# Optimization experiments

Measured on AMD Instinct MI355X. Metric: run time of the kernel, lower is better.

The kernel has to match this reference:

```python
import jax, jax.numpy as jnp
import numpy as np

B, T, C, H = 8, 2048, 1024, 64  # batch, seq (== block_size), n_embd, head_size


def setup_inputs() -> dict:
    key = jax.random.key(0)
    k1, k2, k3, k4 = jax.random.split(key, 4)
    x = jax.random.normal(k1, (B, T, C), dtype=jnp.float32)
    scale = 0.02
    Wk = jax.random.normal(k2, (H, C), dtype=jnp.float32) * scale  # nn.Linear weight [out,in]
    Wq = jax.random.normal(k3, (H, C), dtype=jnp.float32) * scale
    Wv = jax.random.normal(k4, (H, C), dtype=jnp.float32) * scale
    return {"x": x, "Wk": Wk, "Wq": Wq, "Wv": Wv}


def reference(x, Wk, Wq, Wv):
    # k, q, v projections (bias-free linears): x @ W.T
    k = jnp.einsum('btc,hc->bth', x, Wk)
    q = jnp.einsum('btc,hc->bth', x, Wq)
    v = jnp.einsum('btc,hc->bth', x, Wv)
    # NOTE: source MULTIPLIES by sqrt(head_size) (faithful to original code)
    wei = jnp.einsum('bth,bsh->bts', q, k) * (H ** 0.5)  # [B,T,T]
    causal = jnp.tril(jnp.ones((T, T), dtype=bool))
    wei = jnp.where(causal, wei, -jnp.inf)
    wei = jax.nn.softmax(wei, axis=-1)
    # dropout_value = 0.0 -> identity (deterministic baseline)
    out = jnp.einsum('bts,bsh->bth', wei, v)  # [B,T,H]
    return out
```

## Files before the change

kernel.cpp:

```cpp
#include <hip/hip_runtime.h>

#define BB 8
#define TT 2048
#define CC 1024
#define HH 64
#define MM (BB * TT)

typedef _Float16 half8 __attribute__((ext_vector_type(8)));
typedef _Float16 half4 __attribute__((ext_vector_type(4)));
typedef float floatx4 __attribute__((ext_vector_type(4)));

template <int CTRL>
__device__ __forceinline__ float dpp_max_step(float x)
{
    union { float f; int i; } u, v;
    u.f = x;
    v.i = __builtin_amdgcn_update_dpp(u.i, u.i, CTRL, 0xf, 0xf, false);
    return fmaxf(x, v.f);
}
__device__ __forceinline__ float rowmax16(float x)
{
    x = dpp_max_step<0x128>(x);
    x = dpp_max_step<0x124>(x);
    x = dpp_max_step<0x122>(x);
    x = dpp_max_step<0x121>(x);
    return x;
}

__global__ __launch_bounds__(256)
void w_convert(const float* __restrict__ Wk, const float* __restrict__ Wq,
               const float* __restrict__ Wv, _Float16* __restrict__ W16)
{
    const int e = (blockIdx.x * 256 + threadIdx.x) * 8;
    const int row = e >> 10;
    const int c   = e & 1023;
    const int which = row >> 6;
    const float* __restrict__ src = (which == 0) ? Wq : ((which == 1) ? Wk : Wv);
    const float scale = (which == 0) ? 8.0f : 1.0f;
    const int srow = row & 63;
    const float4 a = *reinterpret_cast<const float4*>(&src[srow * 1024 + c]);
    const float4 b = *reinterpret_cast<const float4*>(&src[srow * 1024 + c + 4]);
    const half8 o = { (_Float16)(a.x * scale), (_Float16)(a.y * scale),
                      (_Float16)(a.z * scale), (_Float16)(a.w * scale),
                      (_Float16)(b.x * scale), (_Float16)(b.y * scale),
                      (_Float16)(b.z * scale), (_Float16)(b.w * scale) };
    *reinterpret_cast<half8*>(&W16[e]) = o;
}

__device__ __forceinline__ void qkv_loadA(const float* __restrict__ xrow, int k0,
                                          float4& xa, float4& xb)
{
    xa = *reinterpret_cast<const float4*>(xrow + k0);
    xb = *reinterpret_cast<const float4*>(xrow + k0 + 4);
}
__device__ __forceinline__ void qkv_loadB(const _Float16* __restrict__ wbase, int k0,
                                          half8 (&bf)[12])
{
    #pragma unroll
    for (int n = 0; n < 12; ++n)
        bf[n] = *reinterpret_cast<const half8*>(wbase + (size_t)n * 16 * CC + k0);
}
__device__ __forceinline__ void qkv_mfma(const float4& xa, const float4& xb,
                                         const half8 (&bf)[12], floatx4 (&acc)[12])
{
    const half8 af = { (_Float16)xa.x, (_Float16)xa.y, (_Float16)xa.z, (_Float16)xa.w,
                       (_Float16)xb.x, (_Float16)xb.y, (_Float16)xb.z, (_Float16)xb.w };
    #pragma unroll
    for (int n = 0; n < 12; ++n)
        acc[n] = __builtin_amdgcn_mfma_f32_16x16x32_f16(af, bf[n], acc[n], 0, 0, 0);
}

__global__ __launch_bounds__(256, 1)
void qkv_direct(const float* __restrict__ x, const _Float16* __restrict__ W16,
                _Float16* __restrict__ q16, _Float16* __restrict__ k16,
                _Float16* __restrict__ vt16)
{
    const int tid  = threadIdx.x;
    const int lane = tid & 63;
    const int wv   = tid >> 6;
    const int tile = blockIdx.x * 4 + wv;
    const int m_base = tile * 16;
    const int fm = lane & 15;
    const int fq = lane >> 4;
    const int fk = fq * 8;
    const int fr = fq * 4;

    const float*     __restrict__ xrow  = &x[(size_t)(m_base + fm) * CC + fk];
    const _Float16*  __restrict__ wbase = &W16[(size_t)fm * CC + fk];

    floatx4 acc[12];
    #pragma unroll
    for (int n = 0; n < 12; ++n)
        #pragma unroll
        for (int r = 0; r < 4; ++r) acc[n][r] = 0.0f;

    float4 xa0, xb0, xa1, xb1;
    half8 bf0[12], bf1[12];

    qkv_loadA(xrow, 0, xa0, xb0);
    qkv_loadB(wbase, 0, bf0);

    #pragma unroll 2
    for (int c = 0; c < 32; c += 2) {
        qkv_loadA(xrow, (c + 1) * 32, xa1, xb1);
        qkv_loadB(wbase, (c + 1) * 32, bf1);
        qkv_mfma(xa0, xb0, bf0, acc);
        if (c + 2 < 32) {
            qkv_loadA(xrow, (c + 2) * 32, xa0, xb0);
            qkv_loadB(wbase, (c + 2) * 32, bf0);
        }
        qkv_mfma(xa1, xb1, bf1, acc);
    }

    const int b  = m_base >> 11;
    const int t0 = m_base & 2047;
    #pragma unroll
    for (int n = 0; n < 12; ++n) {
        const int col = n * 16 + fm;
        if (n < 8) {
            _Float16* __restrict__ dst = (n < 4) ? q16 : k16;
            const int h = col & 63;
            #pragma unroll
            for (int r = 0; r < 4; ++r)
                dst[(size_t)(m_base + fr + r) * HH + h] = (_Float16)acc[n][r];
        } else {
            const int h = col - 128;
            const half4 pk = { (_Float16)acc[n][0], (_Float16)acc[n][1],
                               (_Float16)acc[n][2], (_Float16)acc[n][3] };
            *reinterpret_cast<half4*>(
                &vt16[((size_t)b * HH + h) * TT + t0 + fr]) = pk;
        }
    }
}

__global__ __launch_bounds__(128, 3)
void attn(const _Float16* __restrict__ q16, const _Float16* __restrict__ k16,
          const _Float16* __restrict__ vt16, float* __restrict__ out)
{
    __shared__ _Float16 Ks[64 * 72];
    __shared__ _Float16 Vts[64 * 72];
    __shared__ _Float16 Ps[2 * 16 * 72];

    const int bid = blockIdx.x;
    const int b = bid & 7;
    const int g = bid >> 3;
    const int it = (g < 32) ? (63 - g) : (g - 32);
    const int tid  = threadIdx.x;
    const int lane = tid & 63;
    const int wv   = tid >> 6;
    const int fm   = lane & 15;
    const int fk   = (lane >> 4) * 8;
    const int fr   = (lane >> 4) * 4;

    const _Float16* __restrict__ qb  = q16  + (size_t)b * TT * HH;
    const _Float16* __restrict__ kb  = k16  + (size_t)b * TT * HH;
    const _Float16* __restrict__ vtb = vt16 + (size_t)b * HH * TT;

    const int qrow = it * 32 + wv * 16 + fm;
    const half8 qf0 = *reinterpret_cast<const half8*>(&qb[(size_t)qrow * HH + fk]);
    const half8 qf1 = *reinterpret_cast<const half8*>(&qb[(size_t)qrow * HH + 32 + fk]);

    floatx4 O[4], lacc;
    float m_r[4];
    #pragma unroll
    for (int r = 0; r < 4; ++r) {
        m_r[r] = -3.0e38f;
        lacc[r] = 0.0f;
        #pragma unroll
        for (int ht = 0; ht < 4; ++ht) O[ht][r] = 0.0f;
    }

    const half8 ones = { (_Float16)1.f, (_Float16)1.f, (_Float16)1.f, (_Float16)1.f,
                         (_Float16)1.f, (_Float16)1.f, (_Float16)1.f, (_Float16)1.f };

    const int Ji = (it >> 1) + 1;
    const int sr = tid >> 3;
    const int sc = (tid & 7) * 8;

    half8 kr[4], vr[4];
    #pragma unroll
    for (int i = 0; i < 4; ++i) {
        kr[i] = *reinterpret_cast<const half8*>(&kb[(size_t)(sr + i * 16) * HH + sc]);
        vr[i] = *reinterpret_cast<const half8*>(&vtb[(size_t)(sr + i * 16) * TT + sc]);
    }

    for (int j = 0; j < Ji; ++j) {
        __syncthreads();
        #pragma unroll
        for (int i = 0; i < 4; ++i) {
            *reinterpret_cast<half8*>(&Ks[(sr + i * 16) * 72 + sc])  = kr[i];
            *reinterpret_cast<half8*>(&Vts[(sr + i * 16) * 72 + sc]) = vr[i];
        }
        __syncthreads();

        if (j + 1 < Ji) {
            const int jn = (j + 1) * 64;
            #pragma unroll
            for (int i = 0; i < 4; ++i) {
                kr[i] = *reinterpret_cast<const half8*>(&kb[(size_t)(jn + sr + i * 16) * HH + sc]);
                vr[i] = *reinterpret_cast<const half8*>(&vtb[(size_t)(sr + i * 16) * TT + jn + sc]);
            }
        }

        floatx4 sa[4];
        #pragma unroll
        for (int nt = 0; nt < 4; ++nt) {
            #pragma unroll
            for (int r = 0; r < 4; ++r) sa[nt][r] = 0.0f;
            const _Float16* kp = &Ks[(nt * 16 + fm) * 72];
            const half8 b0 = *reinterpret_cast<const half8*>(kp + fk);
            const half8 b1 = *reinterpret_cast<const half8*>(kp + 32 + fk);
            sa[nt] = __builtin_amdgcn_mfma_f32_16x16x32_f16(qf0, b0, sa[nt], 0, 0, 0);
            sa[nt] = __builtin_amdgcn_mfma_f32_16x16x32_f16(qf1, b1, sa[nt], 0, 0, 0);
        }

        if (j == Ji - 1) {
            const int rbase = it * 32 + wv * 16 + fr;
            #pragma unroll
            for (int nt = 0; nt < 4; ++nt) {
                const int col = j * 64 + nt * 16 + fm;
                #pragma unroll
                for (int r = 0; r < 4; ++r)
                    if (col > rbase + r) sa[nt][r] = -3.0e38f;
            }
        }

        #pragma unroll
        for (int r = 0; r < 4; ++r) {
            float mx = fmaxf(fmaxf(sa[0][r], sa[1][r]), fmaxf(sa[2][r], sa[3][r]));
            mx = rowmax16(mx);
            const float mn = fmaxf(m_r[r], mx);
            const float alpha = __expf(m_r[r] - mn);
            m_r[r] = mn;
            _Float16* pp = &Ps[wv * 1152 + (fr + r) * 72 + fm];
            pp[0]  = (_Float16)__expf(sa[0][r] - mn);
            pp[16] = (_Float16)__expf(sa[1][r] - mn);
            pp[32] = (_Float16)__expf(sa[2][r] - mn);
            pp[48] = (_Float16)__expf(sa[3][r] - mn);
            lacc[r] *= alpha;
            O[0][r] *= alpha; O[1][r] *= alpha; O[2][r] *= alpha; O[3][r] *= alpha;
        }
        __syncthreads();

        #pragma unroll
        for (int ch = 0; ch < 2; ++ch) {
            const half8 pa = *reinterpret_cast<const half8*>(
                &Ps[wv * 1152 + fm * 72 + ch * 32 + fk]);
            lacc = __builtin_amdgcn_mfma_f32_16x16x32_f16(pa, ones, lacc, 0, 0, 0);
            #pragma unroll
            for (int ht = 0; ht < 4; ++ht) {
                const half8 vb = *reinterpret_cast<const half8*>(
                    &Vts[(ht * 16 + fm) * 72 + ch * 32 + fk]);
                O[ht] = __builtin_amdgcn_mfma_f32_16x16x32_f16(pa, vb, O[ht], 0, 0, 0);
            }
        }
    }

    #pragma unroll
    for (int r = 0; r < 4; ++r) {
        const float inv = 1.0f / lacc[r];
        const size_t rowoff = (size_t)(b * TT + it * 32 + wv * 16 + fr + r) * HH;
        #pragma unroll
        for (int ht = 0; ht < 4; ++ht)
            out[rowoff + ht * 16 + fm] = O[ht][r] * inv;
    }
}

extern "C" void kernel_launch(void* const* d_in, const int* in_sizes, int n_in,
                              void* d_out, int out_size, void* d_ws, size_t ws_size,
                              hipStream_t stream)
{
    (void)in_sizes; (void)n_in; (void)out_size; (void)ws_size;

    const float* x  = (const float*)d_in[0];
    const float* Wk = (const float*)d_in[1];
    const float* Wq = (const float*)d_in[2];
    const float* Wv = (const float*)d_in[3];
    float* out = (float*)d_out;

    _Float16* q16  = (_Float16*)d_ws;
    _Float16* k16  = q16 + (size_t)MM * HH;
    _Float16* vt16 = k16 + (size_t)MM * HH;
    _Float16* W16  = vt16 + (size_t)MM * HH;

    w_convert<<<dim3(96), dim3(256), 0, stream>>>(Wk, Wq, Wv, W16);
    qkv_direct<<<dim3(256), dim3(256), 0, stream>>>(x, W16, q16, k16, vt16);
    attn<<<dim3(512), dim3(128), 0, stream>>>(q16, k16, vt16, out);
}
```

Baseline: 182.4 us.

## Split QKV projection across wave pairs and make attention waves independent

The projection kernel now gives each wave half of the 192 output columns for a 16-row tile. It stages the x tile through per-wave LDS as fp16, in 64-wide K chunks, and runs twice as many blocks. The attention kernel drops the shared K/V LDS tiles, the prefetch registers and all block barriers. Each wave independently handles a 16-row query tile and reads K and V^T straight from global memory, relying on caches. This removes barrier and LDS staging overhead and raises parallelism. In exchange it loses cross-wave K/V reuse, drops the causal load-balancing order, and may leave tail imbalance and more global and L2 traffic.

```diff
diff --git a/kernel.cpp b/kernel.cpp
--- a/kernel.cpp
+++ b/kernel.cpp
@@ -47,78 +47,63 @@
     *reinterpret_cast<half8*>(&W16[e]) = o;
 }
 
-__device__ __forceinline__ void qkv_loadA(const float* __restrict__ xrow, int k0,
-                                          float4& xa, float4& xb)
-{
-    xa = *reinterpret_cast<const float4*>(xrow + k0);
-    xb = *reinterpret_cast<const float4*>(xrow + k0 + 4);
-}
-__device__ __forceinline__ void qkv_loadB(const _Float16* __restrict__ wbase, int k0,
-                                          half8 (&bf)[12])
-{
-    #pragma unroll
-    for (int n = 0; n < 12; ++n)
-        bf[n] = *reinterpret_cast<const half8*>(wbase + (size_t)n * 16 * CC + k0);
-}
-__device__ __forceinline__ void qkv_mfma(const float4& xa, const float4& xb,
-                                         const half8 (&bf)[12], floatx4 (&acc)[12])
-{
-    const half8 af = { (_Float16)xa.x, (_Float16)xa.y, (_Float16)xa.z, (_Float16)xa.w,
-                       (_Float16)xb.x, (_Float16)xb.y, (_Float16)xb.z, (_Float16)xb.w };
-    #pragma unroll
-    for (int n = 0; n < 12; ++n)
-        acc[n] = __builtin_amdgcn_mfma_f32_16x16x32_f16(af, bf[n], acc[n], 0, 0, 0);
-}
-
-__global__ __launch_bounds__(256, 1)
-void qkv_direct(const float* __restrict__ x, const _Float16* __restrict__ W16,
-                _Float16* __restrict__ q16, _Float16* __restrict__ k16,
-                _Float16* __restrict__ vt16)
-{
+__global__ __launch_bounds__(256, 2)
+void qkv2(const float* __restrict__ x, const _Float16* __restrict__ W16,
+          _Float16* __restrict__ q16, _Float16* __restrict__ k16,
+          _Float16* __restrict__ vt16)
+{
+    __shared__ _Float16 Xs[4 * 16 * 68];
+
     const int tid  = threadIdx.x;
     const int lane = tid & 63;
     const int wv   = tid >> 6;
-    const int tile = blockIdx.x * 4 + wv;
-    const int m_base = tile * 16;
+    const int gw   = blockIdx.x * 4 + wv;
+    const int mtile = gw >> 1;
+    const int nh    = gw & 1;
     const int fm = lane & 15;
     const int fq = lane >> 4;
     const int fk = fq * 8;
     const int fr = fq * 4;
-
-    const float*     __restrict__ xrow  = &x[(size_t)(m_base + fm) * CC + fk];
-    const _Float16*  __restrict__ wbase = &W16[(size_t)fm * CC + fk];
-
-    floatx4 acc[12];
-    #pragma unroll
-    for (int n = 0; n < 12; ++n)
+    const int m_base = mtile * 16;
+
+    _Float16* __restrict__ Xw = &Xs[wv * 16 * 68];
+    const _Float16* __restrict__ wb = &W16[(size_t)(nh * 96 + fm) * CC + fk];
+
+    floatx4 acc[6];
+    #pragma unroll
+    for (int n = 0; n < 6; ++n)
         #pragma unroll
         for (int r = 0; r < 4; ++r) acc[n][r] = 0.0f;
 
-    float4 xa0, xb0, xa1, xb1;
-    half8 bf0[12], bf1[12];
-
-    qkv_loadA(xrow, 0, xa0, xb0);
-    qkv_loadB(wbase, 0, bf0);
-
-    #pragma unroll 2
-    for (int c = 0; c < 32; c += 2) {
-        qkv_loadA(xrow, (c + 1) * 32, xa1, xb1);
-        qkv_loadB(wbase, (c + 1) * 32, bf1);
-        qkv_mfma(xa0, xb0, bf0, acc);
-        if (c + 2 < 32) {
-            qkv_loadA(xrow, (c + 2) * 32, xa0, xb0);
-            qkv_loadB(wbase, (c + 2) * 32, bf0);
-        }
-        qkv_mfma(xa1, xb1, bf1, acc);
+    for (int k0 = 0; k0 < CC; k0 += 64) {
+        #pragma unroll
+        for (int i = 0; i < 4; ++i) {
+            const float4 xv = *reinterpret_cast<const float4*>(
+                &x[(size_t)(m_base + i * 4 + fq) * CC + k0 + fm * 4]);
+            const half4 h = { (_Float16)xv.x, (_Float16)xv.y,
+                              (_Float16)xv.z, (_Float16)xv.w };
+            *reinterpret_cast<half4*>(&Xw[(i * 4 + fq) * 68 + fm * 4]) = h;
+        }
+        const half8 af0 = *reinterpret_cast<const half8*>(&Xw[fm * 68 + fk]);
+        const half8 af1 = *reinterpret_cast<const half8*>(&Xw[fm * 68 + 32 + fk]);
+
+        #pragma unroll
+        for (int n = 0; n < 6; ++n) {
+            const _Float16* wp = wb + (size_t)n * 16 * CC + k0;
+            const half8 b0 = *reinterpret_cast<const half8*>(wp);
+            const half8 b1 = *reinterpret_cast<const half8*>(wp + 32);
+            acc[n] = __builtin_amdgcn_mfma_f32_16x16x32_f16(af0, b0, acc[n], 0, 0, 0);
+            acc[n] = __builtin_amdgcn_mfma_f32_16x16x32_f16(af1, b1, acc[n], 0, 0, 0);
+        }
     }
 
     const int b  = m_base >> 11;
     const int t0 = m_base & 2047;
     #pragma unroll
-    for (int n = 0; n < 12; ++n) {
-        const int col = n * 16 + fm;
-        if (n < 8) {
-            _Float16* __restrict__ dst = (n < 4) ? q16 : k16;
+    for (int n = 0; n < 6; ++n) {
+        const int col = nh * 96 + n * 16 + fm;
+        if (col < 128) {
+            _Float16* __restrict__ dst = (col < 64) ? q16 : k16;
             const int h = col & 63;
             #pragma unroll
             for (int r = 0; r < 4; ++r)
@@ -133,30 +118,29 @@
     }
 }
 
-__global__ __launch_bounds__(128, 3)
+__global__ __launch_bounds__(256, 1)
 void attn(const _Float16* __restrict__ q16, const _Float16* __restrict__ k16,
           const _Float16* __restrict__ vt16, float* __restrict__ out)
 {
-    __shared__ _Float16 Ks[64 * 72];
-    __shared__ _Float16 Vts[64 * 72];
-    __shared__ _Float16 Ps[2 * 16 * 72];
-
-    const int bid = blockIdx.x;
-    const int b = bid & 7;
-    const int g = bid >> 3;
-    const int it = (g < 32) ? (63 - g) : (g - 32);
+    __shared__ _Float16 Ps[4 * 16 * 68];
+
     const int tid  = threadIdx.x;
     const int lane = tid & 63;
     const int wv   = tid >> 6;
-    const int fm   = lane & 15;
-    const int fk   = (lane >> 4) * 8;
-    const int fr   = (lane >> 4) * 4;
+    const int gw   = blockIdx.x * 4 + wv;
+    const int b    = gw >> 7;
+    const int it   = gw & 127;
+    const int fm = lane & 15;
+    const int fq = lane >> 4;
+    const int fk = fq * 8;
+    const int fr = fq * 4;
 
     const _Float16* __restrict__ qb  = q16  + (size_t)b * TT * HH;
     const _Float16* __restrict__ kb  = k16  + (size_t)b * TT * HH;
     const _Float16* __restrict__ vtb = vt16 + (size_t)b * HH * TT;
-
-    const int qrow = it * 32 + wv * 16 + fm;
+    _Float16* __restrict__ Pw = &Ps[wv * 16 * 68];
+
+    const int qrow = it * 16 + fm;
     const half8 qf0 = *reinterpret_cast<const half8*>(&qb[(size_t)qrow * HH + fk]);
     const half8 qf1 = *reinterpret_cast<const half8*>(&qb[(size_t)qrow * HH + 32 + fk]);
 
@@ -169,45 +153,21 @@
         #pragma unroll
         for (int ht = 0; ht < 4; ++ht) O[ht][r] = 0.0f;
     }
-
     const half8 ones = { (_Float16)1.f, (_Float16)1.f, (_Float16)1.f, (_Float16)1.f,
                          (_Float16)1.f, (_Float16)1.f, (_Float16)1.f, (_Float16)1.f };
 
-    const int Ji = (it >> 1) + 1;
-    const int sr = tid >> 3;
-    const int sc = (tid & 7) * 8;
-
-    half8 kr[4], vr[4];
-    #pragma unroll
-    for (int i = 0; i < 4; ++i) {
-        kr[i] = *reinterpret_cast<const half8*>(&kb[(size_t)(sr + i * 16) * HH + sc]);
-        vr[i] = *reinterpret_cast<const half8*>(&vtb[(size_t)(sr + i * 16) * TT + sc]);
-    }
+    const int Ji = (it >> 2) + 1;
 
     for (int j = 0; j < Ji; ++j) {
-        __syncthreads();
-        #pragma unroll
-        for (int i = 0; i < 4; ++i) {
-            *reinterpret_cast<half8*>(&Ks[(sr + i * 16) * 72 + sc])  = kr[i];
-            *reinterpret_cast<half8*>(&Vts[(sr + i * 16) * 72 + sc]) = vr[i];
-        }
-        __syncthreads();
-
-        if (j + 1 < Ji) {
-            const int jn = (j + 1) * 64;
-            #pragma unroll
-            for (int i = 0; i < 4; ++i) {
-                kr[i] = *reinterpret_cast<const half8*>(&kb[(size_t)(jn + sr + i * 16) * HH + sc]);
-                vr[i] = *reinterpret_cast<const half8*>(&vtb[(size_t)(sr + i * 16) * TT + jn + sc]);
-            }
-        }
+        const _Float16* __restrict__ kjb = kb + (size_t)j * 64 * HH;
+        const _Float16* __restrict__ vjb = vtb + j * 64;
 
         floatx4 sa[4];
         #pragma unroll
         for (int nt = 0; nt < 4; ++nt) {
             #pragma unroll
             for (int r = 0; r < 4; ++r) sa[nt][r] = 0.0f;
-            const _Float16* kp = &Ks[(nt * 16 + fm) * 72];
+            const _Float16* kp = kjb + (size_t)(nt * 16 + fm) * HH;
             const half8 b0 = *reinterpret_cast<const half8*>(kp + fk);
             const half8 b1 = *reinterpret_cast<const half8*>(kp + 32 + fk);
             sa[nt] = __builtin_amdgcn_mfma_f32_16x16x32_f16(qf0, b0, sa[nt], 0, 0, 0);
@@ -215,7 +175,7 @@
         }
 
         if (j == Ji - 1) {
-            const int rbase = it * 32 + wv * 16 + fr;
+            const int rbase = it * 16 + fr;
             #pragma unroll
             for (int nt = 0; nt < 4; ++nt) {
                 const int col = j * 64 + nt * 16 + fm;
@@ -232,7 +192,7 @@
             const float mn = fmaxf(m_r[r], mx);
             const float alpha = __expf(m_r[r] - mn);
             m_r[r] = mn;
-            _Float16* pp = &Ps[wv * 1152 + (fr + r) * 72 + fm];
+            _Float16* pp = &Pw[(fr + r) * 68 + fm];
             pp[0]  = (_Float16)__expf(sa[0][r] - mn);
             pp[16] = (_Float16)__expf(sa[1][r] - mn);
             pp[32] = (_Float16)__expf(sa[2][r] - mn);
@@ -240,17 +200,16 @@
             lacc[r] *= alpha;
             O[0][r] *= alpha; O[1][r] *= alpha; O[2][r] *= alpha; O[3][r] *= alpha;
         }
-        __syncthreads();
 
         #pragma unroll
         for (int ch = 0; ch < 2; ++ch) {
             const half8 pa = *reinterpret_cast<const half8*>(
-                &Ps[wv * 1152 + fm * 72 + ch * 32 + fk]);
+                &Pw[fm * 68 + ch * 32 + fk]);
             lacc = __builtin_amdgcn_mfma_f32_16x16x32_f16(pa, ones, lacc, 0, 0, 0);
             #pragma unroll
             for (int ht = 0; ht < 4; ++ht) {
                 const half8 vb = *reinterpret_cast<const half8*>(
-                    &Vts[(ht * 16 + fm) * 72 + ch * 32 + fk]);
+                    &vjb[(size_t)(ht * 16 + fm) * TT + ch * 32 + fk]);
                 O[ht] = __builtin_amdgcn_mfma_f32_16x16x32_f16(pa, vb, O[ht], 0, 0, 0);
             }
         }
@@ -259,7 +218,7 @@
     #pragma unroll
     for (int r = 0; r < 4; ++r) {
         const float inv = 1.0f / lacc[r];
-        const size_t rowoff = (size_t)(b * TT + it * 32 + wv * 16 + fr + r) * HH;
+        const size_t rowoff = (size_t)(b * TT + it * 16 + fr + r) * HH;
         #pragma unroll
         for (int ht = 0; ht < 4; ++ht)
             out[rowoff + ht * 16 + fm] = O[ht][r] * inv;
@@ -284,6 +243,6 @@
     _Float16* W16  = vt16 + (size_t)MM * HH;
 
     w_convert<<<dim3(96), dim3(256), 0, stream>>>(Wk, Wq, Wv, W16);
-    qkv_direct<<<dim3(256), dim3(256), 0, stream>>>(x, W16, q16, k16, vt16);
-    attn<<<dim3(512), dim3(128), 0, stream>>>(q16, k16, vt16, out);
-}
+    qkv2<<<dim3(512), dim3(256), 0, stream>>>(x, W16, q16, k16, vt16);
+    attn<<<dim3(256), dim3(256), 0, stream>>>(q16, k16, vt16, out);
+}
```

After: 198.9 us. +9.0%, slower.
